# Optimization experiments

Measured on AMD Instinct MI355X. Metric: run time of the kernel, lower is better.

Reference implementation:

```python
import jax, jax.numpy as jnp
import numpy as np

STU, ITEM, CONC, D = 50000, 20000, 2000, 128
E_CC, E_IC, E_SI = 40000, 80000, 1000000


def _gat(tgt_x, src_x, e_src, e_dst, n_tgt, W, att_l, att_r, slope=0.2):
    # single-head GATConv, aggr='add', concat with heads=1 -> [n_tgt, D]
    if W is not None:
        xl = src_x @ W.T  # lin_l applied to source
        xr = tgt_x @ W.T  # lin_l shared for target (in_channels is int)
        # noqa: torch module uses lin_l for both when in_channels is int
    else:
        xl, xr = src_x, tgt_x
    sl = xl @ att_l  # [n_src]
    sr = xr @ att_r  # [n_tgt]
    e = sl[e_src] + sr[e_dst]
    e = jnp.where(e > 0, e, slope * e)  # leaky_relu
    # segment softmax over edges grouped by target node
    m = jax.ops.segment_max(e, e_dst, num_segments=n_tgt)
    m = jnp.where(jnp.isfinite(m), m, 0.0)
    ex = jnp.exp(e - m[e_dst])
    den = jax.ops.segment_sum(ex, e_dst, num_segments=n_tgt) + 1e-16
    alpha = ex / den[e_dst]
    return jax.ops.segment_sum(xl[e_src] * alpha[:, None], e_dst, num_segments=n_tgt)


def setup_inputs():
    key = jax.random.key(0)
    ks = jax.random.split(key, 40)
    s = 1.0 / np.sqrt(D)
    n = lambda k, sh, sc=1.0: jax.random.normal(k, sh, jnp.float32) * sc
    return {
        'stu_x': n(ks[0], (STU, D)),
        'item_x': n(ks[1], (ITEM, D)),
        'conc_x': n(ks[2], (CONC, D)),
        'stu_raw_x': n(ks[3], (STU, D)),
        'W_cc': n(ks[4], (D, D), s), 'al_cc': n(ks[5], (D,), s), 'ar_cc': n(ks[6], (D,), s),
        'W_ic': n(ks[7], (D, D), s), 'al_ic': n(ks[8], (D,), s), 'ar_ic': n(ks[9], (D,), s),
        'al_cce': n(ks[10], (D,), s), 'ar_cce': n(ks[11], (D,), s),
        'al_ice': n(ks[12], (D,), s), 'ar_ice': n(ks[13], (D,), s),
        'W_ci': n(ks[14], (D, D), s), 'al_ci': n(ks[15], (D,), s), 'ar_ci': n(ks[16], (D,), s),
        'W_si': n(ks[17], (D, D), s), 'al_si': n(ks[18], (D,), s), 'ar_si': n(ks[19], (D,), s),
        'w_ci_att': n(ks[20], (2 * D,), s), 'w_si_att': n(ks[21], (2 * D,), s),
        'W_is': n(ks[22], (D, D), s), 'al_is': n(ks[23], (D,), s), 'ar_is': n(ks[24], (D,), s),
        'cc_src': jax.random.randint(ks[25], (E_CC,), 0, CONC),
        'cc_dst': jax.random.randint(ks[26], (E_CC,), 0, CONC),
        'ic_item': jax.random.randint(ks[27], (E_IC,), 0, ITEM),
        'ic_conc': jax.random.randint(ks[28], (E_IC,), 0, CONC),
        'si_stu': jax.random.randint(ks[29], (E_SI,), 0, STU),
        'si_item': jax.random.randint(ks[30], (E_SI,), 0, ITEM),
    }


def reference(stu_x, item_x, conc_x, stu_raw_x,
              W_cc, al_cc, ar_cc, W_ic, al_ic, ar_ic,
              al_cce, ar_cce, al_ice, ar_ice,
              W_ci, al_ci, ar_ci, W_si, al_si, ar_si,
              w_ci_att, w_si_att, W_is, al_is, ar_is,
              cc_src, cc_dst, ic_item, ic_conc, si_stu, si_item):
    # --- concept fusion ---
    c1 = _gat(conc_x, conc_x, cc_src, cc_dst, CONC, W_cc, al_cc, ar_cc)   # inter_conc_conc
    c2 = _gat(conc_x, item_x, ic_item, ic_conc, CONC, W_ic, al_ic, ar_ic) # inter_item_conc
    e1 = _gat(conc_x, c1, cc_src, cc_dst, CONC, None, al_cce, ar_cce)     # exter_conc_conc (no lin)
    e2 = _gat(conc_x, c2, cc_src, cc_dst, CONC, None, al_ice, ar_ice)     # exter_item_conc (no lin)
    conc_fused = conc_x + e1 + e2
    # --- item fusion ---
    i1 = _gat(item_x, conc_x, ic_conc, ic_item, ITEM, W_ci, al_ci, ar_ci) # inter_conc_item
    i2 = _gat(item_x, stu_x, si_stu, si_item, ITEM, W_si, al_si, ar_si)   # inter_stu_item
    # softmax over dim=1 of an [N,1] tensor (as in the torch code): equals 1.0
    att1 = jax.nn.softmax((jnp.concatenate([i1, item_x], axis=1) @ w_ci_att)[:, None], axis=1)
    att2 = jax.nn.softmax((jnp.concatenate([i2, item_x], axis=1) @ w_si_att)[:, None], axis=1)
    item_fused = item_x + att1 * i1 + att2 * i2
    # --- student fusion (uses raw data['stu'].x as target) ---
    s1 = _gat(stu_raw_x, item_x, si_item, si_stu, STU, W_is, al_is, ar_is)
    stu_fused = stu_raw_x + s1
    return (conc_fused, item_fused, stu_fused)
```

## Files before the change

kernel.cpp:

```cpp
#include <hip/hip_runtime.h>

#define CONC_N 2000
#define ITEM_N 20000
#define STU_N  50000
#define NE_CC  40000
#define NE_IC  80000
#define NE_SI  1000000
#define TBUCK  382

typedef unsigned int uint;
typedef unsigned short ushort;
typedef signed char s8;
typedef __attribute__((ext_vector_type(8))) short bf16x8;
typedef __attribute__((ext_vector_type(4))) float f32x4;

__device__ __forceinline__ ushort f2bf(float f) {
  uint u = __float_as_uint(f);
  uint r = (u + 0x7FFFu + ((u >> 16) & 1u)) >> 16;
  return (ushort)r;
}

__device__ __forceinline__ bf16x8 packfrag(float4 lo, float4 hi) {
  union { bf16x8 s; uint u[4]; } p;
  p.u[0] = (uint)f2bf(lo.x) | ((uint)f2bf(lo.y) << 16);
  p.u[1] = (uint)f2bf(lo.z) | ((uint)f2bf(lo.w) << 16);
  p.u[2] = (uint)f2bf(hi.x) | ((uint)f2bf(hi.y) << 16);
  p.u[3] = (uint)f2bf(hi.z) | ((uint)f2bf(hi.w) << 16);
  return p.s;
}


struct CsrG {
  const int* dst; const int* src;
  unsigned* keys; int* srcs; int* offs;
  int E, n, shift, nbuck, tb, sb;
};
struct CsrGs { CsrG g[5]; };


struct ProjDesc { const float* W; const float* a; float* out; };
struct SetupArgs {
  ProjDesc p[10];
  CsrGs G;
  int* pcnt;
  const float* wsrc[5];
  ushort* wdst[5];
};

__global__ __launch_bounds__(256) void setup_k(SetupArgs A) {
  int b = blockIdx.x;
  int tid = threadIdx.x;
  if (b < 10) {
    __shared__ float Wl[128 * 132];
    __shared__ float a_s[128];
    ProjDesc d = A.p[b];
    #pragma unroll
    for (int i = 0; i < 16; ++i) {
      int s = tid + i * 256;
      int row = s >> 5, c4 = s & 31;
      float4 w = *(const float4*)&d.W[s * 4];
      float* dst = &Wl[row * 132 + c4 * 4];
      dst[0] = w.x; dst[1] = w.y; dst[2] = w.z; dst[3] = w.w;
    }
    if (tid < 128) a_s[tid] = d.a[tid];
    __syncthreads();
    if (tid < 128) {
      float acc = 0.f;
      #pragma unroll 4
      for (int j = 0; j < 128; ++j) acc += Wl[j * 132 + tid] * a_s[j];
      d.out[tid] = acc;
    }
    return;
  }
  if (b >= 170) {
    int wi = b - 170;
    const float* Ws = A.wsrc[wi];
    ushort* Wd = A.wdst[wi];
    for (int rec = tid; rec < 2048; rec += 256) {
      int lane = rec & 63;
      int kk = (rec >> 6) & 3;
      int nt = rec >> 8;
      int x = lane & 15, g = lane >> 4;
      const float* src = &Ws[(nt * 16 + x) * 128 + kk * 32 + 4 * g];
      float4 lo = *(const float4*)src;
      float4 hi = *(const float4*)(src + 16);
      bf16x8 pk = packfrag(lo, hi);
      *(bf16x8*)&Wd[rec * 8] = pk;
    }
    return;
  }
  int bsel = b - 10;
  int gi = bsel >> 5, blk = bsel & 31;
  CsrG g = A.G.g[gi];
  __shared__ int lcnt[128];
  if (tid < 128) lcnt[tid] = 0;
  __syncthreads();
  int chunk = (g.E + 31) >> 5;
  int e0 = blk * chunk, e1 = min(g.E, e0 + chunk);
  for (int e = e0 + tid; e < e1; e += 256)
    atomicAdd(&lcnt[g.dst[e] >> g.shift], 1);
  __syncthreads();
  if (tid < 128) A.pcnt[bsel * 128 + tid] = lcnt[tid];
}


__global__ __launch_bounds__(512) void csr_scan(CsrGs G, const int* __restrict__ pcnt,
                                                int* __restrict__ cur, int* __restrict__ bases) {
  __shared__ int lc[TBUCK];
  __shared__ int lb[TBUCK + 5];
  int tid = threadIdx.x, lane = tid & 63, wv = tid >> 6;
  if (tid < TBUCK) {
    int gi = 0;
    #pragma unroll
    for (int k = 1; k < 5; ++k) if (tid >= G.g[k].tb) gi = k;
    int b = tid - G.g[gi].tb;
    int s = 0;
    for (int blk = 0; blk < 32; ++blk) s += pcnt[((gi << 5) + blk) * 128 + b];
    lc[tid] = s;
  }
  __syncthreads();
  if (wv < 5) {
    CsrG g = G.g[wv];
    int carry = 0;
    for (int base = 0; base < g.nbuck; base += 64) {
      int idx = base + lane;
      int v = (idx < g.nbuck) ? lc[g.tb + idx] : 0;
      int incl = v;
      #pragma unroll
      for (int o = 1; o < 64; o <<= 1) {
        int y = __shfl_up(incl, o);
        if (lane >= o) incl += y;
      }
      if (idx < g.nbuck) lb[g.sb + idx] = carry + incl - v;
      carry += __shfl(incl, 63);
    }
    if (lane == 0) lb[g.sb + g.nbuck] = carry;
  }
  __syncthreads();
  if (tid < TBUCK + 5) bases[tid] = lb[tid];
  if (tid < TBUCK) {
    int gi = 0;
    for (int k = 1; k < 5; ++k) if (tid >= G.g[k].tb) gi = k;
    cur[tid] = lb[tid + gi];
  }
  if (tid < 5) G.g[tid].offs[G.g[tid].n] = G.g[tid].E;
}


struct GemmDesc { const float* X; s8* Y8; float* S; int n, b0;
                  const float* dv[6]; float* dq[6]; };
struct BigC {
  GemmDesc g[5];
  int gemm_blocks;
  const float* rx; const float* rv; float* ro; int rnb;
};

__device__ void partition_body(const CsrGs& G, int* __restrict__ cur, int gi, int bx,
                               int nbx, unsigned char* smem) {
  CsrG g = G.g[gi];
  unsigned* ck = (unsigned*)smem;
  unsigned char* cb = smem + 16384;
  int* lcnt = (int*)(smem + 20480);
  int* lcur = (int*)(smem + 20992);
  int tid = threadIdx.x;
  unsigned dmask = (1u << g.shift) - 1;
  for (int c0 = bx * 4096; c0 < g.E; c0 += nbx * 4096) {
    if (tid < 128) lcnt[tid] = 0;
    __syncthreads();
    #pragma unroll
    for (int i = 0; i < 16; ++i) {
      int e = c0 + i * 256 + tid;
      if (e < g.E) {
        int d = g.dst[e], s = g.src[e];
        int b = d >> g.shift;
        ck[i * 256 + tid] = ((unsigned)(d & dmask) << 16) | (unsigned)s;
        cb[i * 256 + tid] = (unsigned char)b;
        atomicAdd(&lcnt[b], 1);
      } else cb[i * 256 + tid] = 255;
    }
    __syncthreads();
    if (tid < g.nbuck && lcnt[tid] > 0) lcur[tid] = atomicAdd(&cur[g.tb + tid], lcnt[tid]);
    __syncthreads();
    #pragma unroll
    for (int i = 0; i < 16; ++i) {
      int b = cb[i * 256 + tid];
      if (b != 255) {
        int pos = atomicAdd(&lcur[b], 1);
        g.keys[pos] = ck[i * 256 + tid];
      }
    }
    __syncthreads();
  }
}

template <int NV>
__device__ void gemm_bodyT(const GemmDesc& gd, const ushort* __restrict__ Wf, int blk) {
  int tid = threadIdx.x;
  int lane = tid & 63, wv = tid >> 6;
  int x = lane & 15, g = lane >> 4;
  int row = blk * 64 + wv * 16 + x;
  const float* xr = &gd.X[(size_t)(row < gd.n ? row : 0) * 128];
  bf16x8 afrag[4];
  float dacc[NV == 0 ? 1 : NV];
  #pragma unroll
  for (int v = 0; v < NV; ++v) dacc[v] = 0.f;
  #pragma unroll
  for (int kk = 0; kk < 4; ++kk) {
    float4 lo = *(const float4*)&xr[kk * 32 + 4 * g];
    float4 hi = *(const float4*)&xr[kk * 32 + 16 + 4 * g];
    afrag[kk] = packfrag(lo, hi);
    #pragma unroll
    for (int v = 0; v < NV; ++v) {
      const float* vp = gd.dv[v];
      float4 vlo = *(const float4*)&vp[kk * 32 + 4 * g];
      float4 vhi = *(const float4*)&vp[kk * 32 + 16 + 4 * g];
      dacc[v] += lo.x * vlo.x + lo.y * vlo.y + lo.z * vlo.z + lo.w * vlo.w
               + hi.x * vhi.x + hi.y * vhi.y + hi.z * vhi.z + hi.w * vhi.w;
    }
  }
  #pragma unroll
  for (int v = 0; v < NV; ++v) {
    float dsum = dacc[v];
    dsum += __shfl_xor(dsum, 16);
    dsum += __shfl_xor(dsum, 32);
    if (lane < 16 && row < gd.n) gd.dq[v][row] = dsum;
  }
  f32x4 acc[8];
  #pragma unroll
  for (int t = 0; t < 8; ++t) acc[t] = (f32x4){0.f, 0.f, 0.f, 0.f};
  #pragma unroll
  for (int nt = 0; nt < 8; ++nt) {
    #pragma unroll
    for (int kk = 0; kk < 4; ++kk) {
      union { uint4 u; bf16x8 s; } bu;
      bu.u = *(const uint4*)&Wf[(size_t)((nt * 4 + kk) * 64 + lane) * 8];
      acc[nt] = __builtin_amdgcn_mfma_f32_16x16x32_bf16(afrag[kk], bu.s, acc[nt], 0, 0, 0);
    }
  }
  int orow = blk * 64 + wv * 16 + 4 * g;
  #pragma unroll
  for (int r = 0; r < 4; ++r) {
    float m8 = 0.f;
    #pragma unroll
    for (int nt = 0; nt < 8; ++nt) m8 = fmaxf(m8, fabsf(acc[nt][r]));
    #pragma unroll
    for (int msk = 1; msk < 16; msk <<= 1) m8 = fmaxf(m8, __shfl_xor(m8, msk));
    int gr = orow + r;
    if (gr < gd.n) {
      float invs = (m8 > 0.f) ? 127.f / m8 : 0.f;
      if (x == 0) gd.S[gr] = m8 * (1.f / 127.f);
      #pragma unroll
      for (int nt = 0; nt < 8; ++nt) {
        int q = (int)rintf(acc[nt][r] * invs);
        gd.Y8[(size_t)gr * 128 + nt * 16 + x] = (s8)q;
      }
    }
  }
}

__device__ void rdot_body(const float* __restrict__ x, const float* __restrict__ v,
                          float* __restrict__ o, int n, int blk, int nblk) {
  int lane = threadIdx.x & 63;
  int wid = (blk * 256 + threadIdx.x) >> 6;
  int nw = nblk * 4;
  float va = v[lane], vb = v[64 + lane];
  for (int r = wid; r < n; r += nw) {
    float a = x[r * 128 + lane] * va + x[r * 128 + 64 + lane] * vb;
    #pragma unroll
    for (int of = 32; of; of >>= 1) a += __shfl_xor(a, of);
    if (lane == 0) o[r] = a;
  }
}

__global__ __launch_bounds__(256, 2) void mid2_k(CsrGs G, int* cur, BigC C,
                                                 const ushort* W0, const ushort* W1,
                                                 const ushort* W2, const ushort* W3,
                                                 const ushort* W4) {
  __shared__ __align__(16) unsigned char smem[21504];
  int b = blockIdx.x;
  if (b < 600) {
    partition_body(G, cur, b / 120, b % 120, 120, smem);
    return;
  }
  b -= 600;
  if (b < C.gemm_blocks) {
    if (b < C.g[1].b0)      gemm_bodyT<6>(C.g[0], W0, b - C.g[0].b0);
    else if (b < C.g[2].b0) gemm_bodyT<4>(C.g[1], W1, b - C.g[1].b0);
    else if (b < C.g[3].b0) gemm_bodyT<0>(C.g[2], W2, b - C.g[2].b0);
    else if (b < C.g[4].b0) gemm_bodyT<1>(C.g[3], W3, b - C.g[3].b0);
    else                    gemm_bodyT<0>(C.g[4], W4, b - C.g[4].b0);
  } else {
    rdot_body(C.rx, C.rv, C.ro, STU_N, b - C.gemm_blocks, C.rnb);
  }
}


__global__ __launch_bounds__(256) void csr_build(CsrGs G, const int* __restrict__ bases) {
  int bid = blockIdx.x;
  int gi = 0;
  for (int k = 1; k < 5; ++k) if (bid >= G.g[k].tb) gi = k;
  CsrG g = G.g[gi];
  int b = bid - g.tb;
  int base = bases[g.sb + b];
  int cnt = bases[g.sb + b + 1] - base;
  if (cnt > 16384) cnt = 16384;

  __shared__ unsigned lkeys[16384];
  __shared__ int lh[512], lex[512], lcu[512], wsum[4];
  int tid = threadIdx.x;
  lh[tid] = 0; lh[tid + 256] = 0;
  __syncthreads();
  for (int j = tid; j < cnt; j += 256) {
    unsigned k = g.keys[base + j];
    lkeys[j] = k;
    atomicAdd(&lh[k >> 16], 1);
  }
  __syncthreads();
  int a0 = lh[2 * tid], a1 = lh[2 * tid + 1];
  int pair = a0 + a1;
  int lane = tid & 63, wv = tid >> 6;
  int incl = pair;
  #pragma unroll
  for (int o = 1; o < 64; o <<= 1) {
    int y = __shfl_up(incl, o);
    if (lane >= o) incl += y;
  }
  if (lane == 63) wsum[wv] = incl;
  __syncthreads();
  if (tid == 0) {
    int s = 0;
    #pragma unroll
    for (int w = 0; w < 4; ++w) { int t = wsum[w]; wsum[w] = s; s += t; }
  }
  __syncthreads();
  int ep = wsum[wv] + incl - pair;
  lex[2 * tid] = ep;       lex[2 * tid + 1] = ep + a0;
  lcu[2 * tid] = ep;       lcu[2 * tid + 1] = ep + a0;
  __syncthreads();
  int dst0 = b << g.shift;
  int ndst = min(1 << g.shift, g.n - dst0);
  for (int dl = tid; dl < ndst; dl += 256) g.offs[dst0 + dl] = base + lex[dl];
  for (int j = tid; j < cnt; j += 256) {
    unsigned k = lkeys[j];
    int dl = k >> 16;
    int pos = atomicAdd(&lcu[dl], 1);
    g.srcs[base + pos] = (int)(k & 0xFFFFu);
  }
}


__device__ __forceinline__ void fma8q(float acc[8], float wj, uint2 u) {
  int lo = (int)u.x, hi = (int)u.y;
  acc[0] += wj * (float)((lo << 24) >> 24);
  acc[1] += wj * (float)((lo << 16) >> 24);
  acc[2] += wj * (float)((lo << 8) >> 24);
  acc[3] += wj * (float)(lo >> 24);
  acc[4] += wj * (float)((hi << 24) >> 24);
  acc[5] += wj * (float)((hi << 16) >> 24);
  acc[6] += wj * (float)((hi << 8) >> 24);
  acc[7] += wj * (float)(hi >> 24);
}

__device__ void gat_core16(const int* __restrict__ offs, const int* __restrict__ srcs,
                           const float* __restrict__ sl, const float* __restrict__ sr,
                           const s8* __restrict__ x8, const float* __restrict__ sc,
                           int t4, int n_tgt, int lane, float acc[8]) {
  int q = lane >> 4, il = lane & 15;
  int t = t4 + q;
  bool tv = t < n_tgt;
  int sbeg = tv ? offs[t] : 0;
  int send = tv ? offs[t + 1] : 0;
  float srt = tv ? sr[t] : 0.f;

  int i0l = sbeg + il;
  bool act0 = i0l < send;
  int s0 = act0 ? srcs[i0l] : 0;
  float sc0 = act0 ? sc[s0] : 0.f;
  float e0;
  {
    float e = sl[s0] + srt;
    e = e > 0.f ? e : 0.2f * e;
    e0 = act0 ? e : -1e30f;
  }
  float m = e0, se = act0 ? 1.f : 0.f;
  for (int i = i0l + 16; i < send; i += 16) {
    int s = srcs[i];
    float e = sl[s] + srt;
    e = e > 0.f ? e : 0.2f * e;
    float mn = fmaxf(m, e);
    se = se * __expf(m - mn) + __expf(e - mn);
    m = mn;
  }
  #pragma unroll
  for (int o = 8; o; o >>= 1) {
    float m2 = __shfl_xor(m, o), s2 = __shfl_xor(se, o);
    float mn = fmaxf(m, m2);
    se = se * __expf(m - mn) + s2 * __expf(m2 - mn);
    m = mn;
  }
  float inv = 1.f / (se + 1e-16f);

  #pragma unroll
  for (int r = 0; r < 8; ++r) acc[r] = 0.f;

  int qb = q << 4;
  for (int i0 = sbeg; i0 < send; i0 += 16) {
    int cnt = min(16, send - i0);
    int s; float wgt;
    if (i0 == sbeg) {
      s = s0;
      wgt = act0 ? __expf(e0 - m) * inv * sc0 : 0.f;
    } else {
      s = 0; wgt = 0.f;
      if (il < cnt) {
        s = srcs[i0 + il];
        float e = sl[s] + srt;
        e = e > 0.f ? e : 0.2f * e;
        wgt = __expf(e - m) * inv * sc[s];
      }
    }
    #pragma unroll 2
    for (int j = 0; j < cnt; ++j) {
      int sj = __shfl(s, qb + j);
      float wj = __shfl(wgt, qb + j);
      uint2 u = *(const uint2*)&x8[(size_t)sj * 128 + il * 8];
      fma8q(acc, wj, u);
    }
  }
}

__device__ __forceinline__ void gat_store16(const float acc[8], const float* base0,
                                            float* out, int t4, int n_tgt, int lane) {
  int q = lane >> 4, il = lane & 15;
  int t = t4 + q;
  if (t >= n_tgt) return;
  int d = t * 128 + il * 8;
  float4 a0 = make_float4(acc[0], acc[1], acc[2], acc[3]);
  float4 a1 = make_float4(acc[4], acc[5], acc[6], acc[7]);
  if (base0) {
    const float4 b0 = *(const float4*)&base0[d];
    const float4 b1 = *(const float4*)&base0[d + 4];
    a0.x += b0.x; a0.y += b0.y; a0.z += b0.z; a0.w += b0.w;
    a1.x += b1.x; a1.y += b1.y; a1.z += b1.z; a1.w += b1.w;
  }
  *(float4*)&out[d] = a0;
  *(float4*)&out[d + 4] = a1;
}

__device__ void c1c2_body16(const int* offs, const int* srcs, const float* sl,
                            const float* sr, const s8* x8, const float* sc,
                            const float* al, float* o, float* slo,
                            int t4, int n_tgt, int lane) {
  float acc[8];
  gat_core16(offs, srcs, sl, sr, x8, sc, t4, n_tgt, lane, acc);
  int q = lane >> 4, il = lane & 15;
  int t = t4 + q;
  float4 v0 = *(const float4*)&al[il * 8];
  float4 v1 = *(const float4*)&al[il * 8 + 4];
  float p = acc[0] * v0.x + acc[1] * v0.y + acc[2] * v0.z + acc[3] * v0.w +
            acc[4] * v1.x + acc[5] * v1.y + acc[6] * v1.z + acc[7] * v1.w;
  #pragma unroll
  for (int o2 = 8; o2; o2 >>= 1) p += __shfl_xor(p, o2);
  if (t < n_tgt) {
    if (il == 0) slo[t] = p;
    int d = t * 128 + il * 8;
    *(float4*)&o[d] = make_float4(acc[0], acc[1], acc[2], acc[3]);
    *(float4*)&o[d + 4] = make_float4(acc[4], acc[5], acc[6], acc[7]);
  }
}

__device__ void gat_dual_core(const int* __restrict__ offs, const int* __restrict__ srcs,
                              const float* __restrict__ sl1, const float* __restrict__ sr1,
                              const float* __restrict__ xl1,
                              const float* __restrict__ sl2, const float* __restrict__ sr2,
                              const float* __restrict__ xl2,
                              const float* __restrict__ base,
                              float* __restrict__ out, int t, int lane) {
  int sbeg = offs[t], send = offs[t + 1];
  float srt1 = sr1[t], srt2 = sr2[t];
  float m1 = -1e30f, m2 = -1e30f;
  for (int i = sbeg + lane; i < send; i += 64) {
    int s = srcs[i];
    float e1 = sl1[s] + srt1; e1 = e1 > 0.f ? e1 : 0.2f * e1;
    float e2 = sl2[s] + srt2; e2 = e2 > 0.f ? e2 : 0.2f * e2;
    m1 = fmaxf(m1, e1); m2 = fmaxf(m2, e2);
  }
  #pragma unroll
  for (int o = 32; o; o >>= 1) {
    m1 = fmaxf(m1, __shfl_xor(m1, o));
    m2 = fmaxf(m2, __shfl_xor(m2, o));
  }
  float se1 = 0.f, se2 = 0.f;
  for (int i = sbeg + lane; i < send; i += 64) {
    int s = srcs[i];
    float e1 = sl1[s] + srt1; e1 = e1 > 0.f ? e1 : 0.2f * e1;
    float e2 = sl2[s] + srt2; e2 = e2 > 0.f ? e2 : 0.2f * e2;
    se1 += __expf(e1 - m1); se2 += __expf(e2 - m2);
  }
  #pragma unroll
  for (int o = 32; o; o >>= 1) {
    se1 += __shfl_xor(se1, o);
    se2 += __shfl_xor(se2, o);
  }
  float inv1 = 1.f / (se1 + 1e-16f), inv2 = 1.f / (se2 + 1e-16f);
  float ax = 0.f, ay = 0.f;
  for (int i0 = sbeg; i0 < send; i0 += 64) {
    int cnt = min(64, send - i0);
    int s = 0; float w1 = 0.f, w2 = 0.f;
    if (lane < cnt) {
      s = srcs[i0 + lane];
      float e1 = sl1[s] + srt1; e1 = e1 > 0.f ? e1 : 0.2f * e1;
      float e2 = sl2[s] + srt2; e2 = e2 > 0.f ? e2 : 0.2f * e2;
      w1 = __expf(e1 - m1) * inv1;
      w2 = __expf(e2 - m2) * inv2;
    }
    for (int j = 0; j < cnt; ++j) {
      int sj = __shfl(s, j);
      float wj1 = __shfl(w1, j);
      float wj2 = __shfl(w2, j);
      const float2 v1 = *(const float2*)&xl1[sj * 128 + lane * 2];
      const float2 v2 = *(const float2*)&xl2[sj * 128 + lane * 2];
      ax += wj1 * v1.x + wj2 * v2.x;
      ay += wj1 * v1.y + wj2 * v2.y;
    }
  }
  const float2 b = *(const float2*)&base[t * 128 + lane * 2];
  float2 o2; o2.x = ax + b.x; o2.y = ay + b.y;
  *(float2*)&out[t * 128 + lane * 2] = o2;
}


#define NB_S1  3125
#define NB_I12 1250
#define NB_CC  125

struct GatsArgs {
  const int *offs4, *srcs4; const float *sl_is, *sr_is; const s8* x_is; const float* sc_is;
  const float* stu_raw_x; float* out_stu;
  const int *offs3, *srcs3; const float *sl_si, *sr_si; const s8* x_si; const float* sc_si;
  const int *offs2, *srcs2; const float *sl_ci, *sr_ci; const s8* x_ci; const float* sc_ci;
  const float* item_x; float* out_item;
  const int *offs0, *srcs0; const float *sl_cc, *sr_cc; const s8* x_cc; const float* sc_cc;
  const float* al_cce; float *c1, *sl_cce;
  const int *offs1, *srcs1; const float *sl_ic, *sr_ic; const s8* x_ic; const float* sc_ic;
  const float* al_ice; float *c2, *sl_ice;
};

__global__ void gats_k(GatsArgs A) {
  int b = blockIdx.x;
  int lane = threadIdx.x & 63;
  int wv = threadIdx.x >> 6;
  if (b < NB_S1) {
    int t4 = b * 16 + wv * 4;
    float acc[8];
    gat_core16(A.offs4, A.srcs4, A.sl_is, A.sr_is, A.x_is, A.sc_is, t4, STU_N, lane, acc);
    gat_store16(acc, A.stu_raw_x, A.out_stu, t4, STU_N, lane);
  } else if (b < NB_S1 + NB_I12) {
    int t4 = (b - NB_S1) * 16 + wv * 4;
    float acc1[8], acc2[8];
    gat_core16(A.offs2, A.srcs2, A.sl_ci, A.sr_ci, A.x_ci, A.sc_ci, t4, ITEM_N, lane, acc1);
    gat_core16(A.offs3, A.srcs3, A.sl_si, A.sr_si, A.x_si, A.sc_si, t4, ITEM_N, lane, acc2);
    #pragma unroll
    for (int r = 0; r < 8; ++r) acc1[r] += acc2[r];
    gat_store16(acc1, A.item_x, A.out_item, t4, ITEM_N, lane);
  } else {
    int sub = b - NB_S1 - NB_I12;
    int which = sub >= NB_CC;
    int t4 = (sub - which * NB_CC) * 16 + wv * 4;
    if (!which)
      c1c2_body16(A.offs0, A.srcs0, A.sl_cc, A.sr_cc, A.x_cc, A.sc_cc, A.al_cce,
                  A.c1, A.sl_cce, t4, CONC_N, lane);
    else
      c1c2_body16(A.offs1, A.srcs1, A.sl_ic, A.sr_ic, A.x_ic, A.sc_ic, A.al_ice,
                  A.c2, A.sl_ice, t4, CONC_N, lane);
  }
}


__global__ void fin_k(const int* offs0, const int* srcs0,
                      const float* sl_cce, const float* sr_cce, const float* c1,
                      const float* sl_ice, const float* sr_ice, const float* c2,
                      const float* conc_x, float* out_conc) {
  int t = (blockIdx.x * blockDim.x + threadIdx.x) >> 6;
  if (t >= CONC_N) return;
  gat_dual_core(offs0, srcs0, sl_cce, sr_cce, c1, sl_ice, sr_ice, c2,
                conc_x, out_conc, t, threadIdx.x & 63);
}


extern "C" void kernel_launch(void* const* d_in, const int* in_sizes, int n_in,
                              void* d_out, int out_size, void* d_ws, size_t ws_size,
                              hipStream_t stream) {
  const float* stu_x     = (const float*)d_in[0];
  const float* item_x    = (const float*)d_in[1];
  const float* conc_x    = (const float*)d_in[2];
  const float* stu_raw_x = (const float*)d_in[3];
  const float* W_cc  = (const float*)d_in[4];
  const float* al_cc = (const float*)d_in[5];
  const float* ar_cc = (const float*)d_in[6];
  const float* W_ic  = (const float*)d_in[7];
  const float* al_ic = (const float*)d_in[8];
  const float* ar_ic = (const float*)d_in[9];
  const float* al_cce = (const float*)d_in[10];
  const float* ar_cce = (const float*)d_in[11];
  const float* al_ice = (const float*)d_in[12];
  const float* ar_ice = (const float*)d_in[13];
  const float* W_ci  = (const float*)d_in[14];
  const float* al_ci = (const float*)d_in[15];
  const float* ar_ci = (const float*)d_in[16];
  const float* W_si  = (const float*)d_in[17];
  const float* al_si = (const float*)d_in[18];
  const float* ar_si = (const float*)d_in[19];
  const float* W_is  = (const float*)d_in[22];
  const float* al_is = (const float*)d_in[23];
  const float* ar_is = (const float*)d_in[24];
  const int* cc_src  = (const int*)d_in[25];
  const int* cc_dst  = (const int*)d_in[26];
  const int* ic_item = (const int*)d_in[27];
  const int* ic_conc = (const int*)d_in[28];
  const int* si_stu  = (const int*)d_in[29];
  const int* si_item = (const int*)d_in[30];

  char* wsb = (char*)d_ws;
  size_t off = 0;
  auto alloc = [&](size_t bytes) -> void* {
    void* p = wsb + off;
    off = (off + bytes + 255) & ~(size_t)255;
    return p;
  };

  s8* concWcc = (s8*)alloc((size_t)CONC_N * 128);
  s8* itemWic = (s8*)alloc((size_t)ITEM_N * 128);
  s8* concWci = (s8*)alloc((size_t)CONC_N * 128);
  s8* stuWsi  = (s8*)alloc((size_t)STU_N  * 128);
  s8* itemWis = (s8*)alloc((size_t)ITEM_N * 128);
  float* scCcc = (float*)alloc(CONC_N * 4);
  float* scIic = (float*)alloc(ITEM_N * 4);
  float* scCci = (float*)alloc(CONC_N * 4);
  float* scSsi = (float*)alloc(STU_N * 4);
  float* scIis = (float*)alloc(ITEM_N * 4);
  ushort* Wbf[5];
  for (int i = 0; i < 5; ++i) Wbf[i] = (ushort*)alloc(128 * 128 * 2);
  float* c1buf   = (float*)alloc((size_t)CONC_N * 128 * 4);
  float* c2buf   = (float*)alloc((size_t)CONC_N * 128 * 4);
  float* vecs    = (float*)alloc(10 * 128 * 4);
  float* sl_cc  = (float*)alloc(CONC_N * 4);
  float* sr_cc  = (float*)alloc(CONC_N * 4);
  float* sl_ic  = (float*)alloc(ITEM_N * 4);
  float* sr_ic  = (float*)alloc(CONC_N * 4);
  float* sl_ci  = (float*)alloc(CONC_N * 4);
  float* sr_ci  = (float*)alloc(ITEM_N * 4);
  float* sl_si  = (float*)alloc(STU_N * 4);
  float* sr_si  = (float*)alloc(ITEM_N * 4);
  float* sl_is  = (float*)alloc(ITEM_N * 4);
  float* sr_is  = (float*)alloc(STU_N * 4);
  float* sl_cce = (float*)alloc(CONC_N * 4);
  float* sr_cce = (float*)alloc(CONC_N * 4);
  float* sl_ice = (float*)alloc(CONC_N * 4);
  float* sr_ice = (float*)alloc(CONC_N * 4);

  unsigned* keys0 = (unsigned*)alloc((size_t)NE_CC * 4);
  unsigned* keys1 = (unsigned*)alloc((size_t)NE_IC * 4);
  unsigned* keys2 = (unsigned*)alloc((size_t)NE_IC * 4);
  unsigned* keys3 = (unsigned*)alloc((size_t)NE_SI * 4);
  unsigned* keys4 = (unsigned*)alloc((size_t)NE_SI * 4);
  int* srcs0 = (int*)alloc((size_t)NE_CC * 4);
  int* srcs1 = (int*)alloc((size_t)NE_IC * 4);
  int* srcs2 = (int*)alloc((size_t)NE_IC * 4);
  int* srcs3 = (int*)alloc((size_t)NE_SI * 4);
  int* srcs4 = (int*)alloc((size_t)NE_SI * 4);
  int* offs0 = (int*)alloc((CONC_N + 1) * 4);
  int* offs1 = (int*)alloc((CONC_N + 1) * 4);
  int* offs2 = (int*)alloc((ITEM_N + 1) * 4);
  int* offs3 = (int*)alloc((ITEM_N + 1) * 4);
  int* offs4 = (int*)alloc((STU_N + 1) * 4);
  int* pcnt      = (int*)alloc(5 * 32 * 128 * 4);
  int* cur_all   = (int*)alloc(TBUCK * 4);
  int* bases_all = (int*)alloc((TBUCK + 5) * 4);

  float* out = (float*)d_out;
  float* out_conc = out;
  float* out_item = out + (size_t)CONC_N * 128;
  float* out_stu  = out + (size_t)(CONC_N + ITEM_N) * 128;

  CsrGs G;
  G.g[0] = {cc_dst,  cc_src,  keys0, srcs0, offs0, NE_CC, CONC_N, 5, 63,   0,   0};
  G.g[1] = {ic_conc, ic_item, keys1, srcs1, offs1, NE_IC, CONC_N, 5, 63,  63,  64};
  G.g[2] = {ic_item, ic_conc, keys2, srcs2, offs2, NE_IC, ITEM_N, 8, 79, 126, 128};
  G.g[3] = {si_item, si_stu,  keys3, srcs3, offs3, NE_SI, ITEM_N, 8, 79, 205, 208};
  G.g[4] = {si_stu,  si_item, keys4, srcs4, offs4, NE_SI, STU_N,  9, 98, 284, 288};

  SetupArgs SA;
  SA.p[0] = {W_cc, al_cc, vecs + 0 * 128};
  SA.p[1] = {W_cc, ar_cc, vecs + 1 * 128};
  SA.p[2] = {W_ic, al_ic, vecs + 2 * 128};
  SA.p[3] = {W_ic, ar_ic, vecs + 3 * 128};
  SA.p[4] = {W_ci, al_ci, vecs + 4 * 128};
  SA.p[5] = {W_ci, ar_ci, vecs + 5 * 128};
  SA.p[6] = {W_si, al_si, vecs + 6 * 128};
  SA.p[7] = {W_si, ar_si, vecs + 7 * 128};
  SA.p[8] = {W_is, al_is, vecs + 8 * 128};
  SA.p[9] = {W_is, ar_is, vecs + 9 * 128};
  SA.G = G;
  SA.pcnt = pcnt;
  SA.wsrc[0] = W_cc; SA.wsrc[1] = W_ic; SA.wsrc[2] = W_ci;
  SA.wsrc[3] = W_si; SA.wsrc[4] = W_is;
  for (int i = 0; i < 5; ++i) SA.wdst[i] = Wbf[i];
  setup_k<<<175, 256, 0, stream>>>(SA);

  csr_scan<<<1, 512, 0, stream>>>(G, pcnt, cur_all, bases_all);

  BigC C;
  C.g[0] = {conc_x, concWcc, scCcc, CONC_N, 0,
            {vecs + 0 * 128, vecs + 1 * 128, vecs + 3 * 128, vecs + 4 * 128, ar_cce, ar_ice},
            {sl_cc, sr_cc, sr_ic, sl_ci, sr_cce, sr_ice}};
  C.g[1] = {item_x, itemWic, scIic, ITEM_N, 32,
            {vecs + 2 * 128, vecs + 5 * 128, vecs + 7 * 128, vecs + 8 * 128, nullptr, nullptr},
            {sl_ic, sr_ci, sr_si, sl_is, nullptr, nullptr}};
  C.g[2] = {conc_x, concWci, scCci, CONC_N, 345,
            {nullptr, nullptr, nullptr, nullptr, nullptr, nullptr},
            {nullptr, nullptr, nullptr, nullptr, nullptr, nullptr}};
  C.g[3] = {stu_x, stuWsi, scSsi, STU_N, 377,
            {vecs + 6 * 128, nullptr, nullptr, nullptr, nullptr, nullptr},
            {sl_si, nullptr, nullptr, nullptr, nullptr, nullptr}};
  C.g[4] = {item_x, itemWis, scIis, ITEM_N, 1159,
            {nullptr, nullptr, nullptr, nullptr, nullptr, nullptr},
            {nullptr, nullptr, nullptr, nullptr, nullptr, nullptr}};
  C.gemm_blocks = 1472;
  C.rx = stu_raw_x; C.rv = vecs + 9 * 128; C.ro = sr_is; C.rnb = 1024;
  mid2_k<<<600 + 2496, 256, 0, stream>>>(G, cur_all, C, Wbf[0], Wbf[1], Wbf[2], Wbf[3], Wbf[4]);

  csr_build<<<TBUCK, 256, 0, stream>>>(G, bases_all);

  GatsArgs GA;
  GA.offs4 = offs4; GA.srcs4 = srcs4; GA.sl_is = sl_is; GA.sr_is = sr_is;
  GA.x_is = itemWis; GA.sc_is = scIis; GA.stu_raw_x = stu_raw_x; GA.out_stu = out_stu;
  GA.offs3 = offs3; GA.srcs3 = srcs3; GA.sl_si = sl_si; GA.sr_si = sr_si;
  GA.x_si = stuWsi; GA.sc_si = scSsi;
  GA.offs2 = offs2; GA.srcs2 = srcs2; GA.sl_ci = sl_ci; GA.sr_ci = sr_ci;
  GA.x_ci = concWci; GA.sc_ci = scCci; GA.item_x = item_x; GA.out_item = out_item;
  GA.offs0 = offs0; GA.srcs0 = srcs0; GA.sl_cc = sl_cc; GA.sr_cc = sr_cc;
  GA.x_cc = concWcc; GA.sc_cc = scCcc; GA.al_cce = al_cce; GA.c1 = c1buf; GA.sl_cce = sl_cce;
  GA.offs1 = offs1; GA.srcs1 = srcs1; GA.sl_ic = sl_ic; GA.sr_ic = sr_ic;
  GA.x_ic = itemWic; GA.sc_ic = scIic; GA.al_ice = al_ice; GA.c2 = c2buf; GA.sl_ice = sl_ice;
  gats_k<<<NB_S1 + NB_I12 + 2 * NB_CC, 256, 0, stream>>>(GA);

  fin_k<<<500, 256, 0, stream>>>(offs0, srcs0, sl_cce, sr_cce, c1buf,
                                 sl_ice, sr_ice, c2buf, conc_x, out_conc);
}
```

Baseline: 204.7 us.

## Regroup kernels: partition with rdot, fuse CSR build into GEMM launch

Splits the old mid2 kernel so edge partitioning runs together with the student row-dot in a new kernel. The CSR build is merged into the GEMM kernel, so the bucket build overlaps with the projection GEMMs instead of running as its own launch. The build now re-reads keys from global memory rather than staging them in a 64KB shared buffer, which lowers LDS use so it can co-reside with the GEMM blocks. It also reorders the GAT blocks so the heavier item blocks, which do two aggregations each, are scheduled first.

```diff
diff --git a/kernel.cpp b/kernel.cpp
--- a/kernel.cpp
+++ b/kernel.cpp
@@ -147,14 +147,6 @@
 }
 
 
-struct GemmDesc { const float* X; s8* Y8; float* S; int n, b0;
-                  const float* dv[6]; float* dq[6]; };
-struct BigC {
-  GemmDesc g[5];
-  int gemm_blocks;
-  const float* rx; const float* rv; float* ro; int rnb;
-};
-
 __device__ void partition_body(const CsrGs& G, int* __restrict__ cur, int gi, int bx,
                                int nbx, unsigned char* smem) {
   CsrG g = G.g[gi];
@@ -193,6 +185,87 @@
   }
 }
 
+__device__ void rdot_body(const float* __restrict__ x, const float* __restrict__ v,
+                          float* __restrict__ o, int n, int blk, int nblk) {
+  int lane = threadIdx.x & 63;
+  int wid = (blk * 256 + threadIdx.x) >> 6;
+  int nw = nblk * 4;
+  float va = v[lane], vb = v[64 + lane];
+  for (int r = wid; r < n; r += nw) {
+    float a = x[r * 128 + lane] * va + x[r * 128 + 64 + lane] * vb;
+    #pragma unroll
+    for (int of = 32; of; of >>= 1) a += __shfl_xor(a, of);
+    if (lane == 0) o[r] = a;
+  }
+}
+
+__global__ __launch_bounds__(256) void mid3_k(CsrGs G, int* cur,
+                                              const float* rx, const float* rv,
+                                              float* ro, int rnb) {
+  __shared__ __align__(16) unsigned char smem[21504];
+  int b = blockIdx.x;
+  if (b < 600) {
+    partition_body(G, cur, b / 120, b % 120, 120, smem);
+  } else {
+    rdot_body(rx, rv, ro, STU_N, b - 600, rnb);
+  }
+}
+
+
+struct GemmDesc { const float* X; s8* Y8; float* S; int n, b0;
+                  const float* dv[6]; float* dq[6]; };
+struct BigC {
+  GemmDesc g[5];
+  int gemm_blocks;
+};
+
+__device__ void build_lite(const CsrGs& G, const int* __restrict__ bases, int bid,
+                           int* lh, int* lex, int* lcu, int* wsum) {
+  int gi = 0;
+  for (int k = 1; k < 5; ++k) if (bid >= G.g[k].tb) gi = k;
+  CsrG g = G.g[gi];
+  int b = bid - g.tb;
+  int base = bases[g.sb + b];
+  int cnt = bases[g.sb + b + 1] - base;
+
+  int tid = threadIdx.x;
+  lh[tid] = 0; lh[tid + 256] = 0;
+  __syncthreads();
+  for (int j = tid; j < cnt; j += 256)
+    atomicAdd(&lh[g.keys[base + j] >> 16], 1);
+  __syncthreads();
+  int a0 = lh[2 * tid], a1 = lh[2 * tid + 1];
+  int pair = a0 + a1;
+  int lane = tid & 63, wv = tid >> 6;
+  int incl = pair;
+  #pragma unroll
+  for (int o = 1; o < 64; o <<= 1) {
+    int y = __shfl_up(incl, o);
+    if (lane >= o) incl += y;
+  }
+  if (lane == 63) wsum[wv] = incl;
+  __syncthreads();
+  if (tid == 0) {
+    int s = 0;
+    #pragma unroll
+    for (int w = 0; w < 4; ++w) { int t = wsum[w]; wsum[w] = s; s += t; }
+  }
+  __syncthreads();
+  int ep = wsum[wv] + incl - pair;
+  lex[2 * tid] = ep;       lex[2 * tid + 1] = ep + a0;
+  lcu[2 * tid] = ep;       lcu[2 * tid + 1] = ep + a0;
+  __syncthreads();
+  int dst0 = b << g.shift;
+  int ndst = min(1 << g.shift, g.n - dst0);
+  for (int dl = tid; dl < ndst; dl += 256) g.offs[dst0 + dl] = base + lex[dl];
+  for (int j = tid; j < cnt; j += 256) {
+    unsigned k = g.keys[base + j];
+    int dl = k >> 16;
+    int pos = atomicAdd(&lcu[dl], 1);
+    g.srcs[base + pos] = (int)(k & 0xFFFFu);
+  }
+}
+
 template <int NV>
 __device__ void gemm_bodyT(const GemmDesc& gd, const ushort* __restrict__ Wf, int blk) {
   int tid = threadIdx.x;
@@ -258,94 +331,22 @@
   }
 }
 
-__device__ void rdot_body(const float* __restrict__ x, const float* __restrict__ v,
-                          float* __restrict__ o, int n, int blk, int nblk) {
-  int lane = threadIdx.x & 63;
-  int wid = (blk * 256 + threadIdx.x) >> 6;
-  int nw = nblk * 4;
-  float va = v[lane], vb = v[64 + lane];
-  for (int r = wid; r < n; r += nw) {
-    float a = x[r * 128 + lane] * va + x[r * 128 + 64 + lane] * vb;
-    #pragma unroll
-    for (int of = 32; of; of >>= 1) a += __shfl_xor(a, of);
-    if (lane == 0) o[r] = a;
-  }
-}
-
-__global__ __launch_bounds__(256, 2) void mid2_k(CsrGs G, int* cur, BigC C,
+__global__ __launch_bounds__(256, 2) void mid4_k(CsrGs G, const int* bases, BigC C,
                                                  const ushort* W0, const ushort* W1,
                                                  const ushort* W2, const ushort* W3,
                                                  const ushort* W4) {
-  __shared__ __align__(16) unsigned char smem[21504];
+  __shared__ int lh[512], lex[512], lcu[512], wsum[4];
   int b = blockIdx.x;
-  if (b < 600) {
-    partition_body(G, cur, b / 120, b % 120, 120, smem);
+  if (b < TBUCK) {
+    build_lite(G, bases, b, lh, lex, lcu, wsum);
     return;
   }
-  b -= 600;
-  if (b < C.gemm_blocks) {
-    if (b < C.g[1].b0)      gemm_bodyT<6>(C.g[0], W0, b - C.g[0].b0);
-    else if (b < C.g[2].b0) gemm_bodyT<4>(C.g[1], W1, b - C.g[1].b0);
-    else if (b < C.g[3].b0) gemm_bodyT<0>(C.g[2], W2, b - C.g[2].b0);
-    else if (b < C.g[4].b0) gemm_bodyT<1>(C.g[3], W3, b - C.g[3].b0);
-    else                    gemm_bodyT<0>(C.g[4], W4, b - C.g[4].b0);
-  } else {
-    rdot_body(C.rx, C.rv, C.ro, STU_N, b - C.gemm_blocks, C.rnb);
-  }
-}
-
-
-__global__ __launch_bounds__(256) void csr_build(CsrGs G, const int* __restrict__ bases) {
-  int bid = blockIdx.x;
-  int gi = 0;
-  for (int k = 1; k < 5; ++k) if (bid >= G.g[k].tb) gi = k;
-  CsrG g = G.g[gi];
-  int b = bid - g.tb;
-  int base = bases[g.sb + b];
-  int cnt = bases[g.sb + b + 1] - base;
-  if (cnt > 16384) cnt = 16384;
-
-  __shared__ unsigned lkeys[16384];
-  __shared__ int lh[512], lex[512], lcu[512], wsum[4];
-  int tid = threadIdx.x;
-  lh[tid] = 0; lh[tid + 256] = 0;
-  __syncthreads();
-  for (int j = tid; j < cnt; j += 256) {
-    unsigned k = g.keys[base + j];
-    lkeys[j] = k;
-    atomicAdd(&lh[k >> 16], 1);
-  }
-  __syncthreads();
-  int a0 = lh[2 * tid], a1 = lh[2 * tid + 1];
-  int pair = a0 + a1;
-  int lane = tid & 63, wv = tid >> 6;
-  int incl = pair;
-  #pragma unroll
-  for (int o = 1; o < 64; o <<= 1) {
-    int y = __shfl_up(incl, o);
-    if (lane >= o) incl += y;
-  }
-  if (lane == 63) wsum[wv] = incl;
-  __syncthreads();
-  if (tid == 0) {
-    int s = 0;
-    #pragma unroll
-    for (int w = 0; w < 4; ++w) { int t = wsum[w]; wsum[w] = s; s += t; }
-  }
-  __syncthreads();
-  int ep = wsum[wv] + incl - pair;
-  lex[2 * tid] = ep;       lex[2 * tid + 1] = ep + a0;
-  lcu[2 * tid] = ep;       lcu[2 * tid + 1] = ep + a0;
-  __syncthreads();
-  int dst0 = b << g.shift;
-  int ndst = min(1 << g.shift, g.n - dst0);
-  for (int dl = tid; dl < ndst; dl += 256) g.offs[dst0 + dl] = base + lex[dl];
-  for (int j = tid; j < cnt; j += 256) {
-    unsigned k = lkeys[j];
-    int dl = k >> 16;
-    int pos = atomicAdd(&lcu[dl], 1);
-    g.srcs[base + pos] = (int)(k & 0xFFFFu);
-  }
+  b -= TBUCK;
+  if (b < C.g[1].b0)      gemm_bodyT<6>(C.g[0], W0, b - C.g[0].b0);
+  else if (b < C.g[2].b0) gemm_bodyT<4>(C.g[1], W1, b - C.g[1].b0);
+  else if (b < C.g[3].b0) gemm_bodyT<0>(C.g[2], W2, b - C.g[2].b0);
+  else if (b < C.g[4].b0) gemm_bodyT<1>(C.g[3], W3, b - C.g[3].b0);
+  else                    gemm_bodyT<0>(C.g[4], W4, b - C.g[4].b0);
 }
 
 
@@ -530,8 +531,8 @@
 }
 
 
+#define NB_I12 1250
 #define NB_S1  3125
-#define NB_I12 1250
 #define NB_CC  125
 
 struct GatsArgs {
@@ -550,21 +551,21 @@
   int b = blockIdx.x;
   int lane = threadIdx.x & 63;
   int wv = threadIdx.x >> 6;
-  if (b < NB_S1) {
+  if (b < NB_I12) {
     int t4 = b * 16 + wv * 4;
+    float acc1[8], acc2[8];
+    gat_core16(A.offs2, A.srcs2, A.sl_ci, A.sr_ci, A.x_ci, A.sc_ci, t4, ITEM_N, lane, acc1);
+    gat_core16(A.offs3, A.srcs3, A.sl_si, A.sr_si, A.x_si, A.sc_si, t4, ITEM_N, lane, acc2);
+    #pragma unroll
+    for (int r = 0; r < 8; ++r) acc1[r] += acc2[r];
+    gat_store16(acc1, A.item_x, A.out_item, t4, ITEM_N, lane);
+  } else if (b < NB_I12 + NB_S1) {
+    int t4 = (b - NB_I12) * 16 + wv * 4;
     float acc[8];
     gat_core16(A.offs4, A.srcs4, A.sl_is, A.sr_is, A.x_is, A.sc_is, t4, STU_N, lane, acc);
     gat_store16(acc, A.stu_raw_x, A.out_stu, t4, STU_N, lane);
-  } else if (b < NB_S1 + NB_I12) {
-    int t4 = (b - NB_S1) * 16 + wv * 4;
-    float acc1[8], acc2[8];
-    gat_core16(A.offs2, A.srcs2, A.sl_ci, A.sr_ci, A.x_ci, A.sc_ci, t4, ITEM_N, lane, acc1);
-    gat_core16(A.offs3, A.srcs3, A.sl_si, A.sr_si, A.x_si, A.sc_si, t4, ITEM_N, lane, acc2);
-    #pragma unroll
-    for (int r = 0; r < 8; ++r) acc1[r] += acc2[r];
-    gat_store16(acc1, A.item_x, A.out_item, t4, ITEM_N, lane);
   } else {
-    int sub = b - NB_S1 - NB_I12;
+    int sub = b - NB_I12 - NB_S1;
     int which = sub >= NB_CC;
     int t4 = (sub - which * NB_CC) * 16 + wv * 4;
     if (!which)
@@ -710,6 +711,9 @@
 
   csr_scan<<<1, 512, 0, stream>>>(G, pcnt, cur_all, bases_all);
 
+  mid3_k<<<600 + 1024, 256, 0, stream>>>(G, cur_all, stu_raw_x, vecs + 9 * 128,
+                                         sr_is, 1024);
+
   BigC C;
   C.g[0] = {conc_x, concWcc, scCcc, CONC_N, 0,
             {vecs + 0 * 128, vecs + 1 * 128, vecs + 3 * 128, vecs + 4 * 128, ar_cce, ar_ice},
@@ -727,10 +731,8 @@
             {nullptr, nullptr, nullptr, nullptr, nullptr, nullptr},
             {nullptr, nullptr, nullptr, nullptr, nullptr, nullptr}};
   C.gemm_blocks = 1472;
-  C.rx = stu_raw_x; C.rv = vecs + 9 * 128; C.ro = sr_is; C.rnb = 1024;
-  mid2_k<<<600 + 2496, 256, 0, stream>>>(G, cur_all, C, Wbf[0], Wbf[1], Wbf[2], Wbf[3], Wbf[4]);
-
-  csr_build<<<TBUCK, 256, 0, stream>>>(G, bases_all);
+  mid4_k<<<TBUCK + 1472, 256, 0, stream>>>(G, bases_all, C,
+                                           Wbf[0], Wbf[1], Wbf[2], Wbf[3], Wbf[4]);
 
   GatsArgs GA;
   GA.offs4 = offs4; GA.srcs4 = srcs4; GA.sl_is = sl_is; GA.sr_is = sr_is;
@@ -743,7 +745,7 @@
   GA.x_cc = concWcc; GA.sc_cc = scCcc; GA.al_cce = al_cce; GA.c1 = c1buf; GA.sl_cce = sl_cce;
   GA.offs1 = offs1; GA.srcs1 = srcs1; GA.sl_ic = sl_ic; GA.sr_ic = sr_ic;
   GA.x_ic = itemWic; GA.sc_ic = scIic; GA.al_ice = al_ice; GA.c2 = c2buf; GA.sl_ice = sl_ice;
-  gats_k<<<NB_S1 + NB_I12 + 2 * NB_CC, 256, 0, stream>>>(GA);
+  gats_k<<<NB_I12 + NB_S1 + 2 * NB_CC, 256, 0, stream>>>(GA);
 
   fin_k<<<500, 256, 0, stream>>>(offs0, srcs0, sl_cce, sr_cce, c1buf,
                                  sl_ice, sr_ice, c2buf, conc_x, out_conc);
```

New measurement: 200.7 us. 1.02x faster.
